# Kernel tuning notes

Hardware: AMD Instinct MI355X
Metric: run time of the kernel (lower is better)

The kernel has to match this reference:

```python
import jax, jax.numpy as jnp
import numpy as np

DIM = 64      # channels
HEADS = 2     # num_heads -> head_dim = 32
K = 7         # neighborhood kernel_size (hardcoded in module)
B, H, W = 1, 96, 96
STAGES = 3
HEAD_DIM = DIM // HEADS


def setup_inputs() -> dict:
    key = jax.random.key(0)
    ks = jax.random.split(key, 6)
    x = jax.random.normal(ks[0], (B, DIM, H, W), jnp.float32)
    qkv_w = jax.random.normal(ks[1], (STAGES, 3 * DIM, DIM), jnp.float32) * 0.02
    qkv_b = jnp.zeros((STAGES, 3 * DIM), jnp.float32)
    proj_w = jax.random.normal(ks[2], (STAGES, DIM, DIM), jnp.float32) * 0.02
    proj_b = jnp.zeros((STAGES, DIM), jnp.float32)
    rpb = jax.random.normal(ks[3], (STAGES, HEADS, 2 * K - 1, 2 * K - 1), jnp.float32) * 0.02
    return {"x": x, "qkv_w": qkv_w, "qkv_b": qkv_b, "proj_w": proj_w,
            "proj_b": proj_b, "rpb": rpb}


def _window_idx(n):
    # NATTEN-style clamped sliding windows: each query attends to exactly K keys.
    starts = jnp.clip(jnp.arange(n) - K // 2, 0, n - K)
    idx = starts[:, None] + jnp.arange(K)          # [n, K] absolute key positions
    rel = idx - jnp.arange(n)[:, None] + (K - 1)   # [n, K] rpb index in [0, 2K-2]
    return idx, rel


def _na_stage(x, qkv_w, qkv_b, proj_w, proj_b, rpb, prev_attn):
    # x: [B, H, W, C]
    b, h_, w_, c = x.shape
    qkv = x @ qkv_w.T + qkv_b                                    # [B,H,W,3C]
    qkv = qkv.reshape(b, h_, w_, 3, HEADS, HEAD_DIM)
    qkv = jnp.transpose(qkv, (3, 0, 4, 1, 2, 5))                 # [3,B,h,H,W,d]
    q, k, v = qkv[0], qkv[1], qkv[2]
    scale = HEAD_DIM ** -0.5

    idx_h, rel_h = _window_idx(h_)
    idx_w, rel_w = _window_idx(w_)

    def gather_nb(t):  # t: [B,h,H,W,d] -> [B,h,H,W,K*K,d]
        t = t[:, :, idx_h]                       # [B,h,H,K,W,d]
        t = t[:, :, :, :, idx_w]                 # [B,h,H,K,W,K,d]
        t = jnp.transpose(t, (0, 1, 2, 4, 3, 5, 6))  # [B,h,H,W,K,K,d]
        return t.reshape(b, HEADS, h_, w_, K * K, HEAD_DIM)

    k_nb = gather_nb(k)
    v_nb = gather_nb(v)

    attn = jnp.einsum('bhijd,bhijkd->bhijk', q * scale, k_nb)   # [B,h,H,W,K*K]

    # relative positional bias: rpb[head, rel_h, rel_w]
    bias = rpb[:, rel_h[:, :, None, None], rel_w[None, None, :, :]]  # [h,H,K,W,K]
    bias = jnp.transpose(bias, (0, 1, 3, 2, 4)).reshape(HEADS, h_, w_, K * K)
    attn = attn + bias[None]

    if prev_attn is not None:  # high-order chaining: previous attention map added to logits
        attn = attn + prev_attn

    attn = jax.nn.softmax(attn, axis=-1)
    out = jnp.einsum('bhijk,bhijkd->bhijd', attn, v_nb)          # [B,h,H,W,d]
    out = jnp.transpose(out, (0, 2, 3, 1, 4)).reshape(b, h_, w_, c)
    out = out @ proj_w.T + proj_b
    return out, attn


def reference(x, qkv_w, qkv_b, proj_w, proj_b, rpb):
    xh = jnp.transpose(x, (0, 2, 3, 1))  # NCHW -> NHWC
    attn = None
    for s in range(STAGES):
        xh, attn = _na_stage(xh, qkv_w[s], qkv_b[s], proj_w[s], proj_b[s], rpb[s], attn)
    return jnp.transpose(xh, (0, 3, 1, 2))  # NHWC -> NCHW
```

## Files before the change

### kernel.cpp

```cpp
#include <hip/hip_runtime.h>

#define HW 96
#define NPIX 9216
#define QN 192
#define ASTRIDE 52
#define SCALE 0.17677669529663687f
#define NT 576
#define HALO_N 132

__device__ __forceinline__ int swz(int row, int col) {
    return row * 64 + (col ^ ((row & 7) << 2));
}

__device__ __forceinline__ int halo_pix(int hp, int hr0, int hc0) {
    int hi = (hp * 745) >> 13;
    int hj = hp - hi * 11;
    int gi = hr0 + hi; gi = gi < 0 ? 0 : (gi > 95 ? 95 : gi);
    int gj = hc0 + hj; gj = gj < 0 ? 0 : (gj > 95 ? 95 : gj);
    return gi * HW + gj;
}

__device__ __forceinline__ void qkv_gemm(const float* __restrict__ xs,
                                         const float* __restrict__ ws,
                                         const float* __restrict__ qb,
                                         float* __restrict__ qkv,
                                         int i0, int j0c, int t)
{
    const int pxg = t % 9, jo = t / 9;
    const int jb = jo * 3;
    float acc[2][3];
    #pragma unroll
    for (int jj = 0; jj < 3; ++jj) {
        float bv = qb[jb + jj];
        acc[0][jj] = bv; acc[1][jj] = bv;
    }
    #pragma unroll
    for (int cc = 0; cc < 16; ++cc) {
        float4 xv[2], wv[3];
        #pragma unroll
        for (int ii = 0; ii < 2; ++ii)
            xv[ii] = *(const float4*)&xs[swz(pxg * 2 + ii, cc * 4)];
        #pragma unroll
        for (int jj = 0; jj < 3; ++jj)
            wv[jj] = *(const float4*)&ws[swz(jb + jj, cc * 4)];
        #pragma unroll
        for (int ii = 0; ii < 2; ++ii)
            #pragma unroll
            for (int jj = 0; jj < 3; ++jj) {
                acc[ii][jj] = fmaf(xv[ii].x, wv[jj].x, acc[ii][jj]);
                acc[ii][jj] = fmaf(xv[ii].y, wv[jj].y, acc[ii][jj]);
                acc[ii][jj] = fmaf(xv[ii].z, wv[jj].z, acc[ii][jj]);
                acc[ii][jj] = fmaf(xv[ii].w, wv[jj].w, acc[ii][jj]);
            }
    }
    #pragma unroll
    for (int ii = 0; ii < 2; ++ii) {
        int px = pxg * 2 + ii;
        float* o = qkv + ((i0 + px / 3) * HW + j0c + px % 3) * QN + jb;
        o[0] = acc[ii][0]; o[1] = acc[ii][1]; o[2] = acc[ii][2];
    }
}

__global__ __launch_bounds__(NT, 5) void k_qkv0(const float* __restrict__ x,
                                                const float* __restrict__ qw,
                                                const float* __restrict__ qb,
                                                float* __restrict__ qkv)
{
    __shared__ float xs[18 * 64];
    __shared__ float ws[QN * 64];
    const int t = threadIdx.x;
    const int tile = ((blockIdx.x & 7) << 6) | (blockIdx.x >> 3);
    const int i0 = (tile >> 5) * 6, j0c = (tile & 31) * 3;
    #pragma unroll
    for (int it = 0; it < 2; ++it) {
        int l = it * NT + t;
        int px = l % 18, c = l / 18;
        xs[swz(px, c)] = x[c * NPIX + (i0 + px / 3) * HW + j0c + px % 3];
    }
    #pragma unroll
    for (int it = 0; it < 6; ++it) {
        int l = it * NT + t;
        if (l < 3072) {
            int j = l >> 4, cs = (l & 15) << 2;
            *(float4*)&ws[swz(j, cs)] = *(const float4*)&qw[j * 64 + cs];
        }
    }
    __syncthreads();
    qkv_gemm(xs, ws, qb, qkv, i0, j0c, t);
}

template <int HASPREV, int LAST>
__global__ __launch_bounds__(NT, 5) void k_stage(const float* __restrict__ qkv,
                                                 const float* __restrict__ rpb,
                                                 const float* __restrict__ prev,
                                                 float* __restrict__ cur,
                                                 const float* __restrict__ pw,
                                                 const float* __restrict__ pb,
                                                 const float* __restrict__ qw,
                                                 const float* __restrict__ qb,
                                                 float* __restrict__ qkvn,
                                                 float* __restrict__ outp)
{
    __shared__ float big[12288];
    __shared__ float qs_s[36 * 32];
    __shared__ float att_s[36 * ASTRIDE];
    __shared__ float xs[18 * 64];
    const int t = threadIdx.x;
    const int tile = ((blockIdx.x & 7) << 6) | (blockIdx.x >> 3);
    const int i0 = (tile >> 5) * 6, j0c = (tile & 31) * 3;
    const int hr0 = i0 - 3, hc0 = j0c - 4;

    #pragma unroll
    for (int it = 0; it < 4; ++it) {
        int hp = it * 36 + (t >> 4);
        if (hp < HALO_N) {
            int c4 = (t & 15) << 2;
            *(float4*)&big[swz(hp, c4)] =
                *(const float4*)&qkv[halo_pix(hp, hr0, hc0) * QN + 64 + c4];
        }
    }
    if (t < 288) {
        int gq = t >> 3, dc = (t & 7) << 2;
        int hq = gq & 1, plq = gq >> 1;
        int pq = (i0 + plq / 3) * HW + j0c + plq % 3;
        *(float4*)&qs_s[gq * 32 + dc] = *(const float4*)&qkv[pq * QN + hq * 32 + dc];
    }
    __syncthreads();
    const int ln = t & 15, g = t >> 4;
    const int h = g & 1, pl = g >> 1;
    const int i = i0 + pl / 3, jx = j0c + pl % 3;
    const int p = i * HW + jx;
    int si = i - 3;  si = si < 0 ? 0 : (si > 89 ? 89 : si);
    int sj = jx - 3; sj = sj < 0 ? 0 : (sj > 89 ? 89 : sj);
    const int hbase = (si - hr0) * 11 + (sj - hc0);
    int hofs[4], aa[4], bb[4], okm[4];
    #pragma unroll
    for (int k = 0; k < 4; ++k) {
        int n = (k << 4) | ln;
        okm[k] = (n <= 48);
        int nn = okm[k] ? n : 0;
        int a = (nn * 147) >> 10;
        int b = nn - a * 7;
        aa[k] = a; bb[k] = b;
        hofs[k] = hbase + a * 11 + b;
    }
    float s0 = 0.f, s1 = 0.f, s2 = 0.f, s3 = 0.f;
    #pragma unroll
    for (int dc = 0; dc < 8; ++dc) {
        float4 qv = *(const float4*)&qs_s[g * 32 + dc * 4];
        float4 k0 = *(const float4*)&big[swz(hofs[0], dc * 4)];
        float4 k1 = *(const float4*)&big[swz(hofs[1], dc * 4)];
        float4 k2 = *(const float4*)&big[swz(hofs[2], dc * 4)];
        float4 k3 = *(const float4*)&big[swz(hofs[3], dc * 4)];
        s0 = fmaf(qv.x, k0.x, s0); s0 = fmaf(qv.y, k0.y, s0);
        s0 = fmaf(qv.z, k0.z, s0); s0 = fmaf(qv.w, k0.w, s0);
        s1 = fmaf(qv.x, k1.x, s1); s1 = fmaf(qv.y, k1.y, s1);
        s1 = fmaf(qv.z, k1.z, s1); s1 = fmaf(qv.w, k1.w, s1);
        s2 = fmaf(qv.x, k2.x, s2); s2 = fmaf(qv.y, k2.y, s2);
        s2 = fmaf(qv.z, k2.z, s2); s2 = fmaf(qv.w, k2.w, s2);
        s3 = fmaf(qv.x, k3.x, s3); s3 = fmaf(qv.y, k3.y, s3);
        s3 = fmaf(qv.w, k3.w, s3); s3 = fmaf(qv.z, k3.z, s3);
    }
    float lg[4] = {s0, s1, s2, s3};
    {
        const float* rp = rpb + h * 169;
        const int rbase = (si - i + 6) * 13 + (sj - jx + 6);
        const int gp = p * 2 + h;
        #pragma unroll
        for (int k = 0; k < 4; ++k) {
            float bv = rp[rbase + aa[k] * 13 + bb[k]];
            float pv = 0.f;
            if (HASPREV) pv = prev[gp * ASTRIDE + ((k << 4) | ln)];
            float l2 = fmaf(lg[k], SCALE, bv + (okm[k] ? pv : 0.f));
            lg[k] = okm[k] ? l2 : -1e30f;
        }
    }
    float mx = fmaxf(fmaxf(lg[0], lg[1]), fmaxf(lg[2], lg[3]));
    mx = fmaxf(mx, __shfl_xor(mx, 1));
    mx = fmaxf(mx, __shfl_xor(mx, 2));
    mx = fmaxf(mx, __shfl_xor(mx, 4));
    mx = fmaxf(mx, __shfl_xor(mx, 8));
    float wk[4];
    float sum = 0.f;
    #pragma unroll
    for (int k = 0; k < 4; ++k) { wk[k] = expf(lg[k] - mx); sum += wk[k]; }
    sum += __shfl_xor(sum, 1);
    sum += __shfl_xor(sum, 2);
    sum += __shfl_xor(sum, 4);
    sum += __shfl_xor(sum, 8);
    const float inv = 1.f / sum;
    wk[0] *= inv; wk[1] *= inv; wk[2] *= inv; wk[3] *= inv;
    att_s[g * ASTRIDE + ln]      = wk[0];
    att_s[g * ASTRIDE + 16 + ln] = wk[1];
    att_s[g * ASTRIDE + 32 + ln] = wk[2];
    if (ln == 0) att_s[g * ASTRIDE + 48] = wk[3];
    if (!LAST) {
        const int gp = p * 2 + h;
        if (ln < 12)
            *(float4*)&cur[gp * ASTRIDE + ln * 4] =
                *(const float4*)&att_s[g * ASTRIDE + ln * 4];
        else if (ln == 12)
            cur[gp * ASTRIDE + 48] = att_s[g * ASTRIDE + 48];
    }
    __syncthreads();
    #pragma unroll
    for (int it = 0; it < 4; ++it) {
        int hp = it * 36 + (t >> 4);
        if (hp < HALO_N) {
            int c4 = (t & 15) << 2;
            *(float4*)&big[swz(hp, c4)] =
                *(const float4*)&qkv[halo_pix(hp, hr0, hc0) * QN + 128 + c4];
        }
    }
    __syncthreads();
    {
        const int vcol = h * 32 + ln * 2;
        float a0 = 0.f, a1 = 0.f;
        #pragma unroll
        for (int kk = 0; kk < 12; ++kk) {
            float4 w4 = *(const float4*)&att_s[g * ASTRIDE + kk * 4];
            #pragma unroll
            for (int c = 0; c < 4; ++c) {
                int n = kk * 4 + c;
                int a = n / 7, b = n % 7;
                float w = (c == 0) ? w4.x : (c == 1) ? w4.y : (c == 2) ? w4.z : w4.w;
                float2 v = *(const float2*)&big[swz(hbase + a * 11 + b, vcol)];
                a0 = fmaf(w, v.x, a0); a1 = fmaf(w, v.y, a1);
            }
        }
        float w48 = att_s[g * ASTRIDE + 48];
        float2 v48 = *(const float2*)&big[swz(hbase + 6 * 11 + 6, vcol)];
        a0 = fmaf(w48, v48.x, a0); a1 = fmaf(w48, v48.y, a1);
        *(float2*)&xs[swz(pl, vcol)] = make_float2(a0, a1);
    }
    __syncthreads();
    #pragma unroll
    for (int it = 0; it < 2; ++it) {
        int l = it * NT + t;
        if (l < 1024) {
            int j = l >> 4, cs = (l & 15) << 2;
            *(float4*)&big[swz(j, cs)] = *(const float4*)&pw[j * 64 + cs];
        }
    }
    __syncthreads();
    const int pxg = t % 9, jo = t / 9;
    float pa0 = pb[jo], pa1 = pa0;
    #pragma unroll
    for (int cc = 0; cc < 16; ++cc) {
        float4 xv0 = *(const float4*)&xs[swz(pxg * 2, cc * 4)];
        float4 xv1 = *(const float4*)&xs[swz(pxg * 2 + 1, cc * 4)];
        float4 wv  = *(const float4*)&big[swz(jo, cc * 4)];
        pa0 = fmaf(xv0.x, wv.x, pa0); pa0 = fmaf(xv0.y, wv.y, pa0);
        pa0 = fmaf(xv0.z, wv.z, pa0); pa0 = fmaf(xv0.w, wv.w, pa0);
        pa1 = fmaf(xv1.x, wv.x, pa1); pa1 = fmaf(xv1.y, wv.y, pa1);
        pa1 = fmaf(xv1.z, wv.z, pa1); pa1 = fmaf(xv1.w, wv.w, pa1);
    }
    __syncthreads();
    xs[swz(pxg * 2, jo)]     = pa0;
    xs[swz(pxg * 2 + 1, jo)] = pa1;
    if (!LAST) {
        #pragma unroll
        for (int it = 0; it < 6; ++it) {
            int l = it * NT + t;
            if (l < 3072) {
                int j = l >> 4, cs = (l & 15) << 2;
                *(float4*)&big[swz(j, cs)] = *(const float4*)&qw[j * 64 + cs];
            }
        }
    }
    __syncthreads();
    if (LAST) {
        #pragma unroll
        for (int it = 0; it < 2; ++it) {
            int l = it * NT + t;
            int px = l % 18, c = l / 18;
            outp[c * NPIX + (i0 + px / 3) * HW + j0c + px % 3] = xs[swz(px, c)];
        }
        return;
    }
    qkv_gemm(xs, big, qb, qkvn, i0, j0c, t);
}

extern "C" void kernel_launch(void* const* d_in, const int* in_sizes, int n_in,
                              void* d_out, int out_size, void* d_ws, size_t ws_size,
                              hipStream_t stream)
{
    const float* x   = (const float*)d_in[0];
    const float* qw  = (const float*)d_in[1];
    const float* qb  = (const float*)d_in[2];
    const float* pw  = (const float*)d_in[3];
    const float* pb  = (const float*)d_in[4];
    const float* rpb = (const float*)d_in[5];
    float* out = (float*)d_out;
    float* ws  = (float*)d_ws;

    float* qkvA = ws;
    float* qkvB = qkvA + 1769472;
    float* attA = qkvB + 1769472;
    float* attB = attA + 958464;

    k_qkv0<<<512, NT, 0, stream>>>(x, qw, qb, qkvA);
    k_stage<0, 0><<<512, NT, 0, stream>>>(qkvA, rpb,       nullptr, attA,
                                          pw,        pb,       qw + 12288, qb + 192, qkvB, nullptr);
    k_stage<1, 0><<<512, NT, 0, stream>>>(qkvB, rpb + 338, attA,    attB,
                                          pw + 4096, pb + 64,  qw + 24576, qb + 384, qkvA, nullptr);
    k_stage<1, 1><<<512, NT, 0, stream>>>(qkvA, rpb + 676, attB,    nullptr,
                                          pw + 8192, pb + 128, nullptr,    nullptr,  nullptr, out);
}
```

Before: 156.9 us.

## Prefetch K, V, prev-attention and weights into registers at stage-kernel start

```diff
diff --git a/kernel.cpp b/kernel.cpp
--- a/kernel.cpp
+++ b/kernel.cpp
@@ -21,13 +21,19 @@
 }
 
 __device__ __forceinline__ void qkv_gemm(const float* __restrict__ xs,
-                                         const float* __restrict__ ws,
+                                         const float* __restrict__ wbig,
                                          const float* __restrict__ qb,
                                          float* __restrict__ qkv,
                                          int i0, int j0c, int t)
 {
     const int pxg = t % 9, jo = t / 9;
     const int jb = jo * 3;
+    int wr[3];
+    #pragma unroll
+    for (int jj = 0; jj < 3; ++jj) {
+        int j = jb + jj;
+        wr[jj] = j + (j >= 132 ? 64 : 0);
+    }
     float acc[2][3];
     #pragma unroll
     for (int jj = 0; jj < 3; ++jj) {
@@ -42,7 +48,7 @@
             xv[ii] = *(const float4*)&xs[swz(pxg * 2 + ii, cc * 4)];
         #pragma unroll
         for (int jj = 0; jj < 3; ++jj)
-            wv[jj] = *(const float4*)&ws[swz(jb + jj, cc * 4)];
+            wv[jj] = *(const float4*)&wbig[swz(wr[jj], cc * 4)];
         #pragma unroll
         for (int ii = 0; ii < 2; ++ii)
             #pragma unroll
@@ -86,7 +92,39 @@
         }
     }
     __syncthreads();
-    qkv_gemm(xs, ws, qb, qkv, i0, j0c, t);
+    const int pxg = t % 9, jo = t / 9;
+    const int jb = jo * 3;
+    float acc[2][3];
+    #pragma unroll
+    for (int jj = 0; jj < 3; ++jj) {
+        float bv = qb[jb + jj];
+        acc[0][jj] = bv; acc[1][jj] = bv;
+    }
+    #pragma unroll
+    for (int cc = 0; cc < 16; ++cc) {
+        float4 xv[2], wv[3];
+        #pragma unroll
+        for (int ii = 0; ii < 2; ++ii)
+            xv[ii] = *(const float4*)&xs[swz(pxg * 2 + ii, cc * 4)];
+        #pragma unroll
+        for (int jj = 0; jj < 3; ++jj)
+            wv[jj] = *(const float4*)&ws[swz(jb + jj, cc * 4)];
+        #pragma unroll
+        for (int ii = 0; ii < 2; ++ii)
+            #pragma unroll
+            for (int jj = 0; jj < 3; ++jj) {
+                acc[ii][jj] = fmaf(xv[ii].x, wv[jj].x, acc[ii][jj]);
+                acc[ii][jj] = fmaf(xv[ii].y, wv[jj].y, acc[ii][jj]);
+                acc[ii][jj] = fmaf(xv[ii].z, wv[jj].z, acc[ii][jj]);
+                acc[ii][jj] = fmaf(xv[ii].w, wv[jj].w, acc[ii][jj]);
+            }
+    }
+    #pragma unroll
+    for (int ii = 0; ii < 2; ++ii) {
+        int px = pxg * 2 + ii;
+        float* o = qkv + ((i0 + px / 3) * HW + j0c + px % 3) * QN + jb;
+        o[0] = acc[ii][0]; o[1] = acc[ii][1]; o[2] = acc[ii][2];
+    }
 }
 
 template <int HASPREV, int LAST>
@@ -101,39 +139,103 @@
                                                  float* __restrict__ qkvn,
                                                  float* __restrict__ outp)
 {
-    __shared__ float big[12288];
-    __shared__ float qs_s[36 * 32];
-    __shared__ float att_s[36 * ASTRIDE];
-    __shared__ float xs[18 * 64];
+    __shared__ float smem[16384 + 36 * ASTRIDE + 18 * 64];
+    float* big   = smem;
+    float* att_s = smem + 16384;
+    float* qsx   = smem + 16384 + 36 * ASTRIDE;
+
     const int t = threadIdx.x;
     const int tile = ((blockIdx.x & 7) << 6) | (blockIdx.x >> 3);
     const int i0 = (tile >> 5) * 6, j0c = (tile & 31) * 3;
     const int hr0 = i0 - 3, hc0 = j0c - 4;
 
-    #pragma unroll
-    for (int it = 0; it < 4; ++it) {
-        int hp = it * 36 + (t >> 4);
-        if (hp < HALO_N) {
-            int c4 = (t & 15) << 2;
-            *(float4*)&big[swz(hp, c4)] =
-                *(const float4*)&qkv[halo_pix(hp, hr0, hc0) * QN + 64 + c4];
-        }
-    }
-    if (t < 288) {
-        int gq = t >> 3, dc = (t & 7) << 2;
-        int hq = gq & 1, plq = gq >> 1;
-        int pq = (i0 + plq / 3) * HW + j0c + plq % 3;
-        *(float4*)&qs_s[gq * 32 + dc] = *(const float4*)&qkv[pq * QN + hq * 32 + dc];
-    }
-    __syncthreads();
     const int ln = t & 15, g = t >> 4;
     const int h = g & 1, pl = g >> 1;
     const int i = i0 + pl / 3, jx = j0c + pl % 3;
     const int p = i * HW + jx;
     int si = i - 3;  si = si < 0 ? 0 : (si > 89 ? 89 : si);
     int sj = jx - 3; sj = sj < 0 ? 0 : (sj > 89 ? 89 : sj);
+
+    const int c4 = (t & 15) << 2;
+    int hpix[4], hps[4];
+    #pragma unroll
+    for (int it = 0; it < 4; ++it) {
+        hps[it] = it * 36 + (t >> 4);
+        hpix[it] = halo_pix(hps[it] < HALO_N ? hps[it] : 0, hr0, hc0);
+    }
+    float4 kreg[4];
+    #pragma unroll
+    for (int it = 0; it < 4; ++it)
+        if (hps[it] < HALO_N)
+            kreg[it] = *(const float4*)&qkv[hpix[it] * QN + 64 + c4];
+    float4 qreg;
+    if (t < 288) {
+        int gq = t >> 3, dc = (t & 7) << 2;
+        int plq = gq >> 1;
+        int pq = (i0 + plq / 3) * HW + j0c + plq % 3;
+        qreg = *(const float4*)&qkv[pq * QN + (gq & 1) * 32 + dc];
+    }
+    float4 pwreg[2];
+    #pragma unroll
+    for (int it = 0; it < 2; ++it) {
+        int l = it * NT + t;
+        if (l < 1024)
+            pwreg[it] = *(const float4*)&pw[(l >> 4) * 64 + ((l & 15) << 2)];
+    }
+    float4 qwh[2];
+    if (!LAST) {
+        #pragma unroll
+        for (int it = 0; it < 2; ++it) {
+            int l = it * NT + t;
+            if (l < 960)
+                qwh[it] = *(const float4*)&qw[(132 + (l >> 4)) * 64 + ((l & 15) << 2)];
+        }
+    }
+    float4 vreg[4];
+    #pragma unroll
+    for (int it = 0; it < 4; ++it)
+        if (hps[it] < HALO_N)
+            vreg[it] = *(const float4*)&qkv[hpix[it] * QN + 128 + c4];
+    float pr[4] = {0.f, 0.f, 0.f, 0.f};
+    if (HASPREV) {
+        #pragma unroll
+        for (int k = 0; k < 4; ++k)
+            pr[k] = prev[(p * 2 + h) * ASTRIDE + ((k << 4) | ln)];
+    }
+    float4 qwl[4];
+    if (!LAST) {
+        #pragma unroll
+        for (int it = 0; it < 4; ++it) {
+            int l = it * NT + t;
+            if (l < 2112)
+                qwl[it] = *(const float4*)&qw[(l >> 4) * 64 + ((l & 15) << 2)];
+        }
+    }
+    #pragma unroll
+    for (int it = 0; it < 4; ++it)
+        if (hps[it] < HALO_N)
+            *(float4*)&big[swz(hps[it], c4)] = kreg[it];
+    if (t < 288) {
+        int gq = t >> 3, dc = (t & 7) << 2;
+        *(float4*)&qsx[gq * 32 + dc] = qreg;
+    }
+    #pragma unroll
+    for (int it = 0; it < 2; ++it) {
+        int l = it * NT + t;
+        if (l < 1024)
+            *(float4*)&big[swz(132 + (l >> 4), (l & 15) << 2)] = pwreg[it];
+    }
+    if (!LAST) {
+        #pragma unroll
+        for (int it = 0; it < 2; ++it) {
+            int l = it * NT + t;
+            if (l < 960)
+                *(float4*)&big[swz(196 + (l >> 4), (l & 15) << 2)] = qwh[it];
+        }
+    }
+    __syncthreads();
     const int hbase = (si - hr0) * 11 + (sj - hc0);
-    int hofs[4], aa[4], bb[4], okm[4];
+    int hofs[4], rbidx[4], okm[4];
     #pragma unroll
     for (int k = 0; k < 4; ++k) {
         int n = (k << 4) | ln;
@@ -141,13 +243,13 @@
         int nn = okm[k] ? n : 0;
         int a = (nn * 147) >> 10;
         int b = nn - a * 7;
-        aa[k] = a; bb[k] = b;
         hofs[k] = hbase + a * 11 + b;
+        rbidx[k] = a * 13 + b;
     }
     float s0 = 0.f, s1 = 0.f, s2 = 0.f, s3 = 0.f;
     #pragma unroll
     for (int dc = 0; dc < 8; ++dc) {
-        float4 qv = *(const float4*)&qs_s[g * 32 + dc * 4];
+        float4 qv = *(const float4*)&qsx[g * 32 + dc * 4];
         float4 k0 = *(const float4*)&big[swz(hofs[0], dc * 4)];
         float4 k1 = *(const float4*)&big[swz(hofs[1], dc * 4)];
         float4 k2 = *(const float4*)&big[swz(hofs[2], dc * 4)];
@@ -159,19 +261,16 @@
         s2 = fmaf(qv.x, k2.x, s2); s2 = fmaf(qv.y, k2.y, s2);
         s2 = fmaf(qv.z, k2.z, s2); s2 = fmaf(qv.w, k2.w, s2);
         s3 = fmaf(qv.x, k3.x, s3); s3 = fmaf(qv.y, k3.y, s3);
-        s3 = fmaf(qv.w, k3.w, s3); s3 = fmaf(qv.z, k3.z, s3);
+        s3 = fmaf(qv.z, k3.z, s3); s3 = fmaf(qv.w, k3.w, s3);
     }
     float lg[4] = {s0, s1, s2, s3};
     {
         const float* rp = rpb + h * 169;
         const int rbase = (si - i + 6) * 13 + (sj - jx + 6);
-        const int gp = p * 2 + h;
         #pragma unroll
         for (int k = 0; k < 4; ++k) {
-            float bv = rp[rbase + aa[k] * 13 + bb[k]];
-            float pv = 0.f;
-            if (HASPREV) pv = prev[gp * ASTRIDE + ((k << 4) | ln)];
-            float l2 = fmaf(lg[k], SCALE, bv + (okm[k] ? pv : 0.f));
+            float bv = rp[rbase + rbidx[k]];
+            float l2 = fmaf(lg[k], SCALE, bv + pr[k]);
             lg[k] = okm[k] ? l2 : -1e30f;
         }
     }
@@ -204,14 +303,9 @@
     }
     __syncthreads();
     #pragma unroll
-    for (int it = 0; it < 4; ++it) {
-        int hp = it * 36 + (t >> 4);
-        if (hp < HALO_N) {
-            int c4 = (t & 15) << 2;
-            *(float4*)&big[swz(hp, c4)] =
-                *(const float4*)&qkv[halo_pix(hp, hr0, hc0) * QN + 128 + c4];
-        }
-    }
+    for (int it = 0; it < 4; ++it)
+        if (hps[it] < HALO_N)
+            *(float4*)&big[swz(hps[it], c4)] = vreg[it];
     __syncthreads();
     {
         const int vcol = h * 32 + ln * 2;
@@ -231,54 +325,43 @@
         float w48 = att_s[g * ASTRIDE + 48];
         float2 v48 = *(const float2*)&big[swz(hbase + 6 * 11 + 6, vcol)];
         a0 = fmaf(w48, v48.x, a0); a1 = fmaf(w48, v48.y, a1);
-        *(float2*)&xs[swz(pl, vcol)] = make_float2(a0, a1);
-    }
-    __syncthreads();
-    #pragma unroll
-    for (int it = 0; it < 2; ++it) {
-        int l = it * NT + t;
-        if (l < 1024) {
-            int j = l >> 4, cs = (l & 15) << 2;
-            *(float4*)&big[swz(j, cs)] = *(const float4*)&pw[j * 64 + cs];
-        }
-    }
-    __syncthreads();
+        *(float2*)&qsx[swz(pl, vcol)] = make_float2(a0, a1);
+    }
+    __syncthreads();
+    if (!LAST) {
+        #pragma unroll
+        for (int it = 0; it < 4; ++it) {
+            int l = it * NT + t;
+            if (l < 2112)
+                *(float4*)&big[swz(l >> 4, (l & 15) << 2)] = qwl[it];
+        }
+    }
     const int pxg = t % 9, jo = t / 9;
     float pa0 = pb[jo], pa1 = pa0;
     #pragma unroll
     for (int cc = 0; cc < 16; ++cc) {
-        float4 xv0 = *(const float4*)&xs[swz(pxg * 2, cc * 4)];
-        float4 xv1 = *(const float4*)&xs[swz(pxg * 2 + 1, cc * 4)];
-        float4 wv  = *(const float4*)&big[swz(jo, cc * 4)];
+        float4 xv0 = *(const float4*)&qsx[swz(pxg * 2, cc * 4)];
+        float4 xv1 = *(const float4*)&qsx[swz(pxg * 2 + 1, cc * 4)];
+        float4 wv  = *(const float4*)&big[swz(132 + jo, cc * 4)];
         pa0 = fmaf(xv0.x, wv.x, pa0); pa0 = fmaf(xv0.y, wv.y, pa0);
         pa0 = fmaf(xv0.z, wv.z, pa0); pa0 = fmaf(xv0.w, wv.w, pa0);
         pa1 = fmaf(xv1.x, wv.x, pa1); pa1 = fmaf(xv1.y, wv.y, pa1);
         pa1 = fmaf(xv1.z, wv.z, pa1); pa1 = fmaf(xv1.w, wv.w, pa1);
     }
     __syncthreads();
-    xs[swz(pxg * 2, jo)]     = pa0;
-    xs[swz(pxg * 2 + 1, jo)] = pa1;
-    if (!LAST) {
-        #pragma unroll
-        for (int it = 0; it < 6; ++it) {
-            int l = it * NT + t;
-            if (l < 3072) {
-                int j = l >> 4, cs = (l & 15) << 2;
-                *(float4*)&big[swz(j, cs)] = *(const float4*)&qw[j * 64 + cs];
-            }
-        }
-    }
+    qsx[swz(pxg * 2, jo)]     = pa0;
+    qsx[swz(pxg * 2 + 1, jo)] = pa1;
     __syncthreads();
     if (LAST) {
         #pragma unroll
         for (int it = 0; it < 2; ++it) {
             int l = it * NT + t;
             int px = l % 18, c = l / 18;
-            outp[c * NPIX + (i0 + px / 3) * HW + j0c + px % 3] = xs[swz(px, c)];
+            outp[c * NPIX + (i0 + px / 3) * HW + j0c + px % 3] = qsx[swz(px, c)];
         }
         return;
     }
-    qkv_gemm(xs, big, qb, qkvn, i0, j0c, t);
+    qkv_gemm(qsx, big, qb, qkvn, i0, j0c, t);
 }
 
 extern "C" void kernel_launch(void* const* d_in, const int* in_sizes, int n_in,
```

Measured after the change: 199.1 us. 1.27x slower.
